# Kernel optimization log

Hardware: AMD Instinct MI355X
Metric: run time of the kernel (lower is better)

Reference implementation:

```python
import jax, jax.numpy as jnp
import numpy as np
from jax import lax

N, XD, L, D, R = 32768, 8, 16, 64, 64
HID_E, HID_N, MIX = 256, 512, 32
LOG2PI = float(np.log(2.0 * np.pi))


def setup_inputs() -> dict:
    key = jax.random.key(0)
    ks = jax.random.split(key, 18)
    g = lambda k, shape, s: (jax.random.normal(k, shape, jnp.float32) * s)
    init_std = 0.001
    return {
        "X": jax.random.normal(ks[0], (N, XD, L), jnp.float32),
        "init_w": g(ks[1], (1, R), init_std),
        "cores": g(ks[2], (L, R, D, R), init_std),          # core_list stacked
        "enc1_w": g(ks[3], (HID_E, XD), 1.0 / np.sqrt(XD)),
        "enc1_b": jnp.zeros((HID_E,), jnp.float32),
        "enc2_w": g(ks[4], (D, HID_E), 1.0 / np.sqrt(HID_E)),
        "enc2_b": jnp.zeros((D,), jnp.float32),
        "nade_w1": g(ks[5], (HID_N, R), 1.0 / np.sqrt(R)),
        "nade_b1": jnp.zeros((HID_N,), jnp.float32),
        "nade_w2": g(ks[6], (R, HID_N), 1.0 / np.sqrt(HID_N)),
        "nade_b2": jnp.zeros((R,), jnp.float32),
        "mu_w": g(ks[7], (MIX * XD, R), 1.0 / np.sqrt(R)),
        "mu_b": jnp.zeros((MIX * XD,), jnp.float32),
        "sig_w": g(ks[8], (MIX * XD, R), 1.0 / np.sqrt(R)),
        "sig_b": jnp.zeros((MIX * XD,), jnp.float32),
        "alpha_w": g(ks[9], (MIX, R), 1.0 / np.sqrt(R)),
        "alpha_b": jnp.zeros((MIX,), jnp.float32),
    }


def _encode(x, enc1_w, enc1_b, enc2_w, enc2_b):
    # x: [..., xd] -> [..., d]  (NADE-style input encoder)
    h = jax.nn.relu(x @ enc1_w.T + enc1_b)
    return h @ enc2_w.T + enc2_b


def _phi(x, h, nade_w1, nade_b1, nade_w2, nade_b2,
         mu_w, mu_b, sig_w, sig_b, alpha_w, alpha_b):
    # x: [n, xd], h: [n, r] hidden state -> [n] mixture-of-Gaussians log-density
    n = x.shape[0]
    h = jax.nn.relu(h @ nade_w1.T + nade_b1)
    h = jax.nn.relu(h @ nade_w2.T + nade_b2)
    mu = (h @ mu_w.T + mu_b).reshape(n, MIX, XD)
    log_sig = (h @ sig_w.T + sig_b).reshape(n, MIX, XD)
    sig = jnp.exp(log_sig)
    log_alpha = jax.nn.log_softmax(h @ alpha_w.T + alpha_b, axis=-1)  # [n, MIX]
    z = (x[:, None, :] - mu) / sig
    comp_lp = jnp.sum(-0.5 * z * z - log_sig - 0.5 * LOG2PI, axis=-1)  # [n, MIX]
    return jax.nn.logsumexp(log_alpha + comp_lp, axis=-1)


def reference(X, init_w, cores, enc1_w, enc1_b, enc2_w, enc2_b,
              nade_w1, nade_b1, nade_w2, nade_b2,
              mu_w, mu_b, sig_w, sig_b, alpha_w, alpha_b):
    n = X.shape[0]
    xseq = jnp.transpose(X, (2, 0, 1))                      # [L, n, xd]
    enc_all = _encode(xseq, enc1_w, enc1_b, enc2_w, enc2_b)  # [L, n, d]
    phi = lambda x, h: _phi(x, h, nade_w1, nade_b1, nade_w2, nade_b2,
                            mu_w, mu_b, sig_w, sig_b, alpha_w, alpha_b)

    tmp0 = jnp.broadcast_to(init_w, (n, R))
    res0 = phi(xseq[0], tmp0)
    norm0 = jnp.sum(tmp0 * tmp0)

    def step(tmp, inp):
        enc_prev, core_prev, x_cur = inp
        tmp = jnp.einsum('nd,ni,idj->nj', enc_prev, tmp, core_prev)
        return tmp, (phi(x_cur, tmp), jnp.sum(tmp * tmp))

    xs = (enc_all[:L - 1], cores[:L - 1], xseq[1:])
    _, (res_steps, norm_steps) = lax.scan(step, tmp0, xs)
    result = res0 + jnp.sum(res_steps, axis=0)   # [n] log-likelihood
    norm = norm0 + jnp.sum(norm_steps)           # scalar Frobenius norm accumulator
    return result, norm
```

## Files before the change

### kernel.cpp

```cpp
#include <hip/hip_runtime.h>

typedef unsigned short u16;
typedef unsigned int u32;
typedef __attribute__((ext_vector_type(8))) __bf16 bf16x8;
typedef __attribute__((ext_vector_type(4))) float f32x4;

#define NSAMP 32768
#define HALF_LOG2PI 0.91893853320467274f

#define O_W1N 0
#define O_W2N 32768
#define O_MUW 65536
#define O_SGW 81920
#define O_ALW 98304
#define O_E1W 100352
#define O_E2W 108544
#define O_CORT 124928
#define CORT_STEP 262144

#define L_TMP 0
#define L_ENC 8192
#define L_H1A 24576
#define L_H1B 32768
#define L_CLP 24576
#define L_ALP 32768
#define L_H2  40960
#define L_LM1 40960
#define L_LM2 41984
#define L_LS1 43008
#define L_LS2 44032
#define L_XP  49152
#define LDS_BYTES 53248

static __device__ __forceinline__ u16 f2b(float x){ return __builtin_bit_cast(u16,(__bf16)x); }
static __device__ __forceinline__ float b2f(u16 u){ return __builtin_bit_cast(float,((u32)u)<<16); }
static __device__ __forceinline__ float b2flo(u32 v){ return __builtin_bit_cast(float, v<<16); }
static __device__ __forceinline__ float b2fhi(u32 v){ return __builtin_bit_cast(float, v & 0xffff0000u); }
static __device__ __forceinline__ u32 pk2(float lo, float hi){
  return (u32)__builtin_bit_cast(u16,(__bf16)lo) | ((u32)__builtin_bit_cast(u16,(__bf16)hi)<<16);
}
static __device__ __forceinline__ f32x4 MF(uint4 a, uint4 b, f32x4 c){
  union U{uint4 q; bf16x8 v;};
  U A, B; A.q=a; B.q=b;
  return __builtin_amdgcn_mfma_f32_16x16x32_bf16(A.v, B.v, c, 0, 0, 0);
}

__global__ void prep_w(const float* __restrict__ nw1, const float* __restrict__ nw2,
                       const float* __restrict__ muw, const float* __restrict__ sgw,
                       const float* __restrict__ alw, const float* __restrict__ e1w,
                       const float* __restrict__ e2w, u16* __restrict__ ws,
                       float* __restrict__ out) {
  int idx0 = blockIdx.x * blockDim.x + threadIdx.x;
  int stride = gridDim.x * blockDim.x;
  for (int idx = idx0; idx < 124928; idx += stride) {
    float v;
    if      (idx < 32768)  v = nw1[idx];
    else if (idx < 65536)  v = nw2[idx - 32768];
    else if (idx < 81920)  v = muw[idx - 65536];
    else if (idx < 98304)  v = sgw[idx - 81920];
    else if (idx < 100352) v = alw[idx - 98304];
    else if (idx < 108544) { int j = idx - 100352; int o = j >> 5, k = j & 31;
                             v = (k < 8) ? e1w[o*8 + k] : 0.0f; }
    else                   v = e2w[idx - 108544];
    ws[idx] = f2b(v);
  }
  if (idx0 == 0) out[NSAMP] = 0.0f;
}

__global__ void prep_core(const float* __restrict__ cores, u16* __restrict__ ws) {
  int t = blockIdx.x >> 6, d = blockIdx.x & 63;
  __shared__ float T[64][65];
  for (int idx = threadIdx.x; idx < 4096; idx += 256) {
    int i = idx >> 6, j = idx & 63;
    T[i][j] = cores[((size_t)(t*64 + i)*64 + d)*64 + j];
  }
  __syncthreads();
  u16* dst = ws + O_CORT + (size_t)t*CORT_STEP + (size_t)d*4096;
  for (int idx = threadIdx.x; idx < 4096; idx += 256) {
    int j = idx >> 6, i = idx & 63;
    dst[j*64 + i] = f2b(T[i][j]);
  }
}

__global__ __launch_bounds__(256, 3)
void fused(const float* __restrict__ X, const float* __restrict__ init_w,
           const float* __restrict__ b1e, const float* __restrict__ b2e,
           const float* __restrict__ b1n, const float* __restrict__ b2n,
           const float* __restrict__ mub, const float* __restrict__ sgb,
           const float* __restrict__ alb, const u16* __restrict__ ws,
           float* __restrict__ out) {
  __shared__ __align__(16) char Lp[LDS_BYTES];
  const int tid = threadIdx.x;
  const int w = tid >> 6, l = tid & 63, li = l & 15, g = l >> 4;
  const int e3 = li & 7;
  const int sw = e3 << 4;
  const int n0 = blockIdx.x * 64;
  float res = 0.f, nrm = 0.f;

  for (int idx = tid; idx < 4096; idx += 256) {
    int s = idx >> 6, r = idx & 63;
    *(u16*)(Lp + L_TMP + s*128 + ((2*r) ^ ((s & 7) << 4))) = f2b(init_w[r]);
  }
  { uint4 z = {0,0,0,0};
    *(uint4*)(Lp + L_XP + tid*16) = z; }
  if (tid < 64) { float v = init_w[tid]; nrm += 64.f * v * v; }
  __syncthreads();

  for (int t = 0; t < 16; ++t) {
    for (int idx = tid; idx < 512; idx += 256) {
      int d = idx >> 6, s = idx & 63;
      float x = X[(size_t)(n0 + s)*128 + d*16 + t];
      *(u16*)(Lp + L_XP + s*64 + ((2*d) ^ ((s & 3) << 4))) = f2b(x);
    }

    uint4 Bq0[4], Bq1[4];
#pragma unroll
    for (int st = 0; st < 4; ++st) {
      int s = st*16 + li;
      Bq0[st] = *(const uint4*)(Lp + L_TMP + s*128 + ((16*g) ^ sw));
      Bq1[st] = *(const uint4*)(Lp + L_TMP + s*128 + ((64 + 16*g) ^ sw));
    }

    f32x4 acc2[4];
#pragma unroll
    for (int st = 0; st < 4; ++st) acc2[st] = (f32x4){0.f,0.f,0.f,0.f};
#pragma unroll 1
    for (int p = 0; p <= 8; ++p) {
      if (p < 8) {
        const u16* a0p = ws + O_W1N + (p*64 + w*16 + li)*64 + 8*g;
        uint4 af0 = *(const uint4*)a0p;
        uint4 af1 = *(const uint4*)(a0p + 32);
        float4 bb = *(const float4*)(b1n + p*64 + w*16 + 4*g);
        char* H1b = Lp + ((p & 1) ? L_H1B : L_H1A);
#pragma unroll
        for (int st = 0; st < 4; ++st) {
          int s = st*16 + li;
          f32x4 a1 = (f32x4){0.f,0.f,0.f,0.f};
          a1 = MF(af0, Bq0[st], a1); a1 = MF(af1, Bq1[st], a1);
          float v0 = fmaxf(a1[0] + bb.x, 0.f), v1 = fmaxf(a1[1] + bb.y, 0.f);
          float v2 = fmaxf(a1[2] + bb.z, 0.f), v3 = fmaxf(a1[3] + bb.w, 0.f);
          *(u32*)(H1b + s*128 + ((32*w + 8*g) ^ sw))     = pk2(v0, v1);
          *(u32*)(H1b + s*128 + ((32*w + 8*g + 4) ^ sw)) = pk2(v2, v3);
        }
      }
      if (p > 0) {
        int q = p - 1;
        const u16* a2p = ws + O_W2N + (w*16 + li)*512 + q*64 + 8*g;
        uint4 c0 = *(const uint4*)a2p;
        uint4 c1 = *(const uint4*)(a2p + 32);
        const char* H1r = Lp + ((q & 1) ? L_H1B : L_H1A);
#pragma unroll
        for (int st = 0; st < 4; ++st) {
          int s = st*16 + li;
          uint4 b0 = *(const uint4*)(H1r + s*128 + ((16*g) ^ sw));
          uint4 b1 = *(const uint4*)(H1r + s*128 + ((64 + 16*g) ^ sw));
          acc2[st] = MF(c0, b0, acc2[st]); acc2[st] = MF(c1, b1, acc2[st]);
        }
      }
      __syncthreads();
    }
    {
      float4 bb = *(const float4*)(b2n + w*16 + 4*g);
#pragma unroll
      for (int st = 0; st < 4; ++st) {
        int s = st*16 + li;
        float v0 = fmaxf(acc2[st][0] + bb.x, 0.f), v1 = fmaxf(acc2[st][1] + bb.y, 0.f);
        float v2 = fmaxf(acc2[st][2] + bb.z, 0.f), v3 = fmaxf(acc2[st][3] + bb.w, 0.f);
        *(u32*)(Lp + L_H2 + s*128 + ((32*w + 8*g) ^ sw))     = pk2(v0, v1);
        *(u32*)(Lp + L_H2 + s*128 + ((32*w + 8*g + 4) ^ sw)) = pk2(v2, v3);
      }
    }
    __syncthreads();

    float xv[4][4];
#pragma unroll
    for (int st = 0; st < 4; ++st) {
      int s = st*16 + li;
      uint2 xq = *(const uint2*)(Lp + L_XP + s*64 + ((8*(g & 1)) ^ ((li & 3) << 4)));
      xv[st][0] = b2flo(xq.x); xv[st][1] = b2fhi(xq.x);
      xv[st][2] = b2flo(xq.y); xv[st][3] = b2fhi(xq.y);
    }

#pragma unroll 1
    for (int c = 0; c < 4; ++c) {
      int ob = c*64 + w*16;
      const u16* as_ = ws + O_SGW + (ob + li)*64 + 8*g;
      const u16* am_ = ws + O_MUW + (ob + li)*64 + 8*g;
      uint4 sf0 = *(const uint4*)as_, sf1 = *(const uint4*)(as_ + 32);
      uint4 mf0 = *(const uint4*)am_, mf1 = *(const uint4*)(am_ + 32);
      float4 bs = *(const float4*)(sgb + ob + 4*g);
      float4 bm = *(const float4*)(mub + ob + 4*g);
      const float bsv[4] = {bs.x,bs.y,bs.z,bs.w};
      const float bmv[4] = {bm.x,bm.y,bm.z,bm.w};
#pragma unroll
      for (int st = 0; st < 4; ++st) {
        int s = st*16 + li;
        uint4 b0 = *(const uint4*)(Lp + L_H2 + s*128 + ((16*g) ^ sw));
        uint4 b1 = *(const uint4*)(Lp + L_H2 + s*128 + ((64 + 16*g) ^ sw));
        f32x4 aS = (f32x4){0.f,0.f,0.f,0.f}, aM = (f32x4){0.f,0.f,0.f,0.f};
        aS = MF(sf0, b0, aS); aS = MF(sf1, b1, aS);
        aM = MF(mf0, b0, aM); aM = MF(mf1, b1, aM);
        float part = 0.f;
#pragma unroll
        for (int r = 0; r < 4; ++r) {
          float ls = aS[r] + bsv[r];
          float mu = aM[r] + bmv[r];
          float z = (xv[st][r] - mu) * __expf(-ls);
          part += -0.5f*z*z - ls - HALF_LOG2PI;
        }
        float comb = part + __shfl_xor(part, 16);
        if (!(g & 1)) {
          int mix = c*8 + 2*w + (g >> 1);
          *(float*)(Lp + L_CLP + (mix*64 + s)*4) = comb;
        }
      }
    }
    {
      int s = w*16 + li;
      uint4 b0 = *(const uint4*)(Lp + L_H2 + s*128 + ((16*g) ^ sw));
      uint4 b1 = *(const uint4*)(Lp + L_H2 + s*128 + ((64 + 16*g) ^ sw));
#pragma unroll
      for (int ot = 0; ot < 2; ++ot) {
        const u16* aa = ws + O_ALW + (ot*16 + li)*64 + 8*g;
        uint4 a0 = *(const uint4*)aa, a1 = *(const uint4*)(aa + 32);
        f32x4 acc = (f32x4){0.f,0.f,0.f,0.f};
        acc = MF(a0, b0, acc); acc = MF(a1, b1, acc);
        float4 ab4 = *(const float4*)(alb + ot*16 + 4*g);
        const float abv[4] = {ab4.x, ab4.y, ab4.z, ab4.w};
#pragma unroll
        for (int r = 0; r < 4; ++r)
          *(float*)(Lp + L_ALP + ((ot*16 + 4*g + r)*64 + s)*4) = acc[r] + abv[r];
      }
    }
    __syncthreads();

    float g1, g2;
    {
      int s = l;
      float m1 = -1e30f, m2 = -1e30f;
#pragma unroll
      for (int mm = 0; mm < 8; ++mm) {
        int m = w*8 + mm;
        float a = *(const float*)(Lp + L_ALP + (m*64 + s)*4);
        float c = *(const float*)(Lp + L_CLP + (m*64 + s)*4);
        m1 = fmaxf(m1, a + c); m2 = fmaxf(m2, a);
      }
      *(float*)(Lp + L_LM1 + (w*64 + s)*4) = m1;
      *(float*)(Lp + L_LM2 + (w*64 + s)*4) = m2;
      __syncthreads();
      g1 = fmaxf(fmaxf(*(const float*)(Lp + L_LM1 + s*4),
                       *(const float*)(Lp + L_LM1 + (64 + s)*4)),
                 fmaxf(*(const float*)(Lp + L_LM1 + (128 + s)*4),
                       *(const float*)(Lp + L_LM1 + (192 + s)*4)));
      g2 = fmaxf(fmaxf(*(const float*)(Lp + L_LM2 + s*4),
                       *(const float*)(Lp + L_LM2 + (64 + s)*4)),
                 fmaxf(*(const float*)(Lp + L_LM2 + (128 + s)*4),
                       *(const float*)(Lp + L_LM2 + (192 + s)*4)));
      float s1 = 0.f, s2 = 0.f;
#pragma unroll
      for (int mm = 0; mm < 8; ++mm) {
        int m = w*8 + mm;
        float a = *(const float*)(Lp + L_ALP + (m*64 + s)*4);
        float c = *(const float*)(Lp + L_CLP + (m*64 + s)*4);
        s1 += __expf(a + c - g1); s2 += __expf(a - g2);
      }
      *(float*)(Lp + L_LS1 + (w*64 + s)*4) = s1;
      *(float*)(Lp + L_LS2 + (w*64 + s)*4) = s2;
      __syncthreads();
    }
    if (tid < 64) {
      float s1 = *(const float*)(Lp + L_LS1 + tid*4)
               + *(const float*)(Lp + L_LS1 + (64 + tid)*4)
               + *(const float*)(Lp + L_LS1 + (128 + tid)*4)
               + *(const float*)(Lp + L_LS1 + (192 + tid)*4);
      float s2 = *(const float*)(Lp + L_LS2 + tid*4)
               + *(const float*)(Lp + L_LS2 + (64 + tid)*4)
               + *(const float*)(Lp + L_LS2 + (128 + tid)*4)
               + *(const float*)(Lp + L_LS2 + (192 + tid)*4);
      res += (g1 + __logf(s1)) - (g2 + __logf(s2));
    }
    if (t == 15) break;
    __syncthreads();

    f32x4 acE[4];
#pragma unroll
    for (int st = 0; st < 4; ++st) acE[st] = (f32x4){0.f,0.f,0.f,0.f};
#pragma unroll 1
    for (int p = 0; p <= 4; ++p) {
      if (p < 4) {
        const u16* aep = ws + O_E1W + (p*64 + w*16 + li)*32 + 8*g;
        uint4 ae = *(const uint4*)aep;
        float4 bb = *(const float4*)(b1e + p*64 + w*16 + 4*g);
        char* H1b = Lp + ((p & 1) ? L_H1B : L_H1A);
#pragma unroll
        for (int st = 0; st < 4; ++st) {
          int s = st*16 + li;
          uint4 b0 = *(const uint4*)(Lp + L_XP + s*64 + ((16*g) ^ ((s & 3) << 4)));
          f32x4 ah = (f32x4){0.f,0.f,0.f,0.f};
          ah = MF(ae, b0, ah);
          float v0 = fmaxf(ah[0] + bb.x, 0.f), v1 = fmaxf(ah[1] + bb.y, 0.f);
          float v2 = fmaxf(ah[2] + bb.z, 0.f), v3 = fmaxf(ah[3] + bb.w, 0.f);
          *(u32*)(H1b + s*128 + ((32*w + 8*g) ^ sw))     = pk2(v0, v1);
          *(u32*)(H1b + s*128 + ((32*w + 8*g + 4) ^ sw)) = pk2(v2, v3);
        }
      }
      if (p > 0) {
        int q = p - 1;
        const u16* c0p = ws + O_E2W + (w*16 + li)*256 + q*64 + 8*g;
        uint4 c0 = *(const uint4*)c0p, c1 = *(const uint4*)(c0p + 32);
        const char* H1r = Lp + ((q & 1) ? L_H1B : L_H1A);
#pragma unroll
        for (int st = 0; st < 4; ++st) {
          int s = st*16 + li;
          uint4 b0 = *(const uint4*)(H1r + s*128 + ((16*g) ^ sw));
          uint4 b1 = *(const uint4*)(H1r + s*128 + ((64 + 16*g) ^ sw));
          acE[st] = MF(c0, b0, acE[st]); acE[st] = MF(c1, b1, acE[st]);
        }
      }
      if (p == 4) {
        float4 be = *(const float4*)(b2e + w*16 + 4*g);
        const float bev[4] = {be.x, be.y, be.z, be.w};
#pragma unroll
        for (int st = 0; st < 4; ++st) {
          int s = st*16 + li;
#pragma unroll
          for (int r = 0; r < 4; ++r) {
            int d = w*16 + 4*g + r;
            *(float*)(Lp + L_ENC + s*256 + ((((d >> 3) ^ e3)) << 5) + ((d & 7) << 2))
                = acE[st][r] + bev[r];
          }
        }
      }
      __syncthreads();
    }

    f32x4 acc[4];
#pragma unroll
    for (int st = 0; st < 4; ++st) acc[st] = (f32x4){0.f,0.f,0.f,0.f};
    const u16* AJ = ws + O_CORT + (size_t)t*CORT_STEP + (size_t)(w*16 + li)*64 + 8*g;
    uint4 Ac0 = *(const uint4*)(AJ);
    uint4 Ac1 = *(const uint4*)(AJ + 32);
#pragma unroll 1
    for (int dg = 0; dg < 16; ++dg) {
      f32x4 E[4];
#pragma unroll
      for (int st = 0; st < 4; ++st)
        E[st] = *(const f32x4*)(Lp + L_ENC + (st*16 + li)*256 +
                                (((dg >> 1) ^ e3) << 5) + ((dg & 1) << 4));
#pragma unroll
      for (int dd = 0; dd < 4; ++dd) {
        uint4 An0 = Ac0, An1 = Ac1;
        if (dd < 3 || dg < 15) {
          const u16* ap = AJ + (size_t)(dg*4 + dd + 1)*4096;
          An0 = *(const uint4*)(ap);
          An1 = *(const uint4*)(ap + 32);
        }
        __builtin_amdgcn_s_setprio(1);
#pragma unroll
        for (int st = 0; st < 4; ++st) {
          f32x4 y = (f32x4){0.f,0.f,0.f,0.f};
          y = MF(Ac0, Bq0[st], y);
          y = MF(Ac1, Bq1[st], y);
          float e = E[st][dd];
          acc[st][0] += e * y[0]; acc[st][1] += e * y[1];
          acc[st][2] += e * y[2]; acc[st][3] += e * y[3];
        }
        __builtin_amdgcn_s_setprio(0);
        Ac0 = An0; Ac1 = An1;
      }
    }
#pragma unroll
    for (int st = 0; st < 4; ++st) {
      int s = st*16 + li;
      nrm += acc[st][0]*acc[st][0] + acc[st][1]*acc[st][1]
           + acc[st][2]*acc[st][2] + acc[st][3]*acc[st][3];
      uint2 pv;
      pv.x = pk2(acc[st][0], acc[st][1]);
      pv.y = pk2(acc[st][2], acc[st][3]);
      *(uint2*)(Lp + L_TMP + s*128 + ((32*w + 8*g) ^ sw)) = pv;
    }
    __syncthreads();
  }

  if (tid < 64) out[n0 + tid] = res;

  __syncthreads();
  *(float*)(Lp + L_H1A + tid*4) = nrm;
  __syncthreads();
  if (tid < 64) {
    float v = *(const float*)(Lp + L_H1A + tid*4)
            + *(const float*)(Lp + L_H1A + (tid + 64)*4)
            + *(const float*)(Lp + L_H1A + (tid + 128)*4)
            + *(const float*)(Lp + L_H1A + (tid + 192)*4);
#pragma unroll
    for (int off = 32; off > 0; off >>= 1) v += __shfl_down(v, off);
    if (tid == 0) atomicAdd(out + NSAMP, v);
  }
}

extern "C" void kernel_launch(void* const* d_in, const int* in_sizes, int n_in,
                              void* d_out, int out_size, void* d_ws, size_t ws_size,
                              hipStream_t stream) {
  const float* X      = (const float*)d_in[0];
  const float* init_w = (const float*)d_in[1];
  const float* cores  = (const float*)d_in[2];
  const float* e1w    = (const float*)d_in[3];
  const float* b1e    = (const float*)d_in[4];
  const float* e2w    = (const float*)d_in[5];
  const float* b2e    = (const float*)d_in[6];
  const float* nw1    = (const float*)d_in[7];
  const float* b1n    = (const float*)d_in[8];
  const float* nw2    = (const float*)d_in[9];
  const float* b2n    = (const float*)d_in[10];
  const float* muw    = (const float*)d_in[11];
  const float* mub    = (const float*)d_in[12];
  const float* sgw    = (const float*)d_in[13];
  const float* sgb    = (const float*)d_in[14];
  const float* alw    = (const float*)d_in[15];
  const float* alb    = (const float*)d_in[16];
  float* out = (float*)d_out;
  u16*   ws  = (u16*)d_ws;

  prep_w<<<64, 256, 0, stream>>>(nw1, nw2, muw, sgw, alw, e1w, e2w, ws, out);
  prep_core<<<960, 256, 0, stream>>>(cores, ws);
  fused<<<NSAMP/64, 256, 0, stream>>>(X, init_w, b1e, b2e, b1n, b2n,
                                      mub, sgb, alb, ws, out);
}
```

Before: 906.0 us.

## Split fused block across 8 waves, halving per-wave sample tiles

Doubles the block to 512 threads so each of 8 waves handles 32 samples (half the sample tiles) instead of 64, with waves split by output slice and sample half. Alpha weights and biases are hoisted out of the time loop into registers. The core contraction loop now double-buffers core fragments two steps ahead and prefetches the next encoder chunk. This raises wave-level parallelism and latency hiding, but each core fragment is now loaded by twice as many waves and the reductions span more partial rows.

```diff
diff --git a/kernel.cpp b/kernel.cpp
--- a/kernel.cpp
+++ b/kernel.cpp
@@ -26,9 +26,9 @@
 #define L_ALP 32768
 #define L_H2  40960
 #define L_LM1 40960
-#define L_LM2 41984
-#define L_LS1 43008
-#define L_LS2 44032
+#define L_LM2 43008
+#define L_LS1 45056
+#define L_LS2 47104
 #define L_XP  49152
 #define LDS_BYTES 53248
 
@@ -82,7 +82,7 @@
   }
 }
 
-__global__ __launch_bounds__(256, 3)
+__global__ __launch_bounds__(512, 4)
 void fused(const float* __restrict__ X, const float* __restrict__ init_w,
            const float* __restrict__ b1e, const float* __restrict__ b2e,
            const float* __restrict__ b1n, const float* __restrict__ b2n,
@@ -92,98 +92,106 @@
   __shared__ __align__(16) char Lp[LDS_BYTES];
   const int tid = threadIdx.x;
   const int w = tid >> 6, l = tid & 63, li = l & 15, g = l >> 4;
+  const int wo = w & 3, wh = w >> 2;
   const int e3 = li & 7;
   const int sw = e3 << 4;
   const int n0 = blockIdx.x * 64;
   float res = 0.f, nrm = 0.f;
 
-  for (int idx = tid; idx < 4096; idx += 256) {
+  uint4 aw0, aw1; float4 ab4;
+  {
+    const u16* aa = ws + O_ALW + (wh*16 + li)*64 + 8*g;
+    aw0 = *(const uint4*)aa; aw1 = *(const uint4*)(aa + 32);
+    ab4 = *(const float4*)(alb + wh*16 + 4*g);
+  }
+  const float4 b2nv = *(const float4*)(b2n + wo*16 + 4*g);
+  const float4 b2ev = *(const float4*)(b2e + wo*16 + 4*g);
+
+  for (int idx = tid; idx < 4096; idx += 512) {
     int s = idx >> 6, r = idx & 63;
     *(u16*)(Lp + L_TMP + s*128 + ((2*r) ^ ((s & 7) << 4))) = f2b(init_w[r]);
   }
-  { uint4 z = {0,0,0,0};
-    *(uint4*)(Lp + L_XP + tid*16) = z; }
+  if (tid < 256) { uint4 z = {0,0,0,0}; *(uint4*)(Lp + L_XP + tid*16) = z; }
   if (tid < 64) { float v = init_w[tid]; nrm += 64.f * v * v; }
   __syncthreads();
 
   for (int t = 0; t < 16; ++t) {
-    for (int idx = tid; idx < 512; idx += 256) {
-      int d = idx >> 6, s = idx & 63;
+    {
+      int d = tid >> 6, s = tid & 63;
       float x = X[(size_t)(n0 + s)*128 + d*16 + t];
       *(u16*)(Lp + L_XP + s*64 + ((2*d) ^ ((s & 3) << 4))) = f2b(x);
     }
 
-    uint4 Bq0[4], Bq1[4];
-#pragma unroll
-    for (int st = 0; st < 4; ++st) {
-      int s = st*16 + li;
-      Bq0[st] = *(const uint4*)(Lp + L_TMP + s*128 + ((16*g) ^ sw));
-      Bq1[st] = *(const uint4*)(Lp + L_TMP + s*128 + ((64 + 16*g) ^ sw));
-    }
-
-    f32x4 acc2[4];
-#pragma unroll
-    for (int st = 0; st < 4; ++st) acc2[st] = (f32x4){0.f,0.f,0.f,0.f};
+    uint4 Bq0[2], Bq1[2];
+#pragma unroll
+    for (int stl = 0; stl < 2; ++stl) {
+      int s = wh*32 + stl*16 + li;
+      Bq0[stl] = *(const uint4*)(Lp + L_TMP + s*128 + ((16*g) ^ sw));
+      Bq1[stl] = *(const uint4*)(Lp + L_TMP + s*128 + ((64 + 16*g) ^ sw));
+    }
+
+    f32x4 acc2[2];
+#pragma unroll
+    for (int stl = 0; stl < 2; ++stl) acc2[stl] = (f32x4){0.f,0.f,0.f,0.f};
 #pragma unroll 1
     for (int p = 0; p <= 8; ++p) {
       if (p < 8) {
-        const u16* a0p = ws + O_W1N + (p*64 + w*16 + li)*64 + 8*g;
+        const u16* a0p = ws + O_W1N + (p*64 + wo*16 + li)*64 + 8*g;
         uint4 af0 = *(const uint4*)a0p;
         uint4 af1 = *(const uint4*)(a0p + 32);
-        float4 bb = *(const float4*)(b1n + p*64 + w*16 + 4*g);
+        float4 bb = *(const float4*)(b1n + p*64 + wo*16 + 4*g);
         char* H1b = Lp + ((p & 1) ? L_H1B : L_H1A);
 #pragma unroll
-        for (int st = 0; st < 4; ++st) {
-          int s = st*16 + li;
+        for (int stl = 0; stl < 2; ++stl) {
+          int s = wh*32 + stl*16 + li;
           f32x4 a1 = (f32x4){0.f,0.f,0.f,0.f};
-          a1 = MF(af0, Bq0[st], a1); a1 = MF(af1, Bq1[st], a1);
+          a1 = MF(af0, Bq0[stl], a1); a1 = MF(af1, Bq1[stl], a1);
           float v0 = fmaxf(a1[0] + bb.x, 0.f), v1 = fmaxf(a1[1] + bb.y, 0.f);
           float v2 = fmaxf(a1[2] + bb.z, 0.f), v3 = fmaxf(a1[3] + bb.w, 0.f);
-          *(u32*)(H1b + s*128 + ((32*w + 8*g) ^ sw))     = pk2(v0, v1);
-          *(u32*)(H1b + s*128 + ((32*w + 8*g + 4) ^ sw)) = pk2(v2, v3);
+          *(u32*)(H1b + s*128 + ((32*wo + 8*g) ^ sw))     = pk2(v0, v1);
+          *(u32*)(H1b + s*128 + ((32*wo + 8*g + 4) ^ sw)) = pk2(v2, v3);
         }
       }
       if (p > 0) {
         int q = p - 1;
-        const u16* a2p = ws + O_W2N + (w*16 + li)*512 + q*64 + 8*g;
+        const u16* a2p = ws + O_W2N + (wo*16 + li)*512 + q*64 + 8*g;
         uint4 c0 = *(const uint4*)a2p;
         uint4 c1 = *(const uint4*)(a2p + 32);
         const char* H1r = Lp + ((q & 1) ? L_H1B : L_H1A);
 #pragma unroll
-        for (int st = 0; st < 4; ++st) {
-          int s = st*16 + li;
+        for (int stl = 0; stl < 2; ++stl) {
+          int s = wh*32 + stl*16 + li;
           uint4 b0 = *(const uint4*)(H1r + s*128 + ((16*g) ^ sw));
           uint4 b1 = *(const uint4*)(H1r + s*128 + ((64 + 16*g) ^ sw));
-          acc2[st] = MF(c0, b0, acc2[st]); acc2[st] = MF(c1, b1, acc2[st]);
+          acc2[stl] = MF(c0, b0, acc2[stl]); acc2[stl] = MF(c1, b1, acc2[stl]);
         }
       }
       __syncthreads();
     }
     {
-      float4 bb = *(const float4*)(b2n + w*16 + 4*g);
-#pragma unroll
-      for (int st = 0; st < 4; ++st) {
-        int s = st*16 + li;
-        float v0 = fmaxf(acc2[st][0] + bb.x, 0.f), v1 = fmaxf(acc2[st][1] + bb.y, 0.f);
-        float v2 = fmaxf(acc2[st][2] + bb.z, 0.f), v3 = fmaxf(acc2[st][3] + bb.w, 0.f);
-        *(u32*)(Lp + L_H2 + s*128 + ((32*w + 8*g) ^ sw))     = pk2(v0, v1);
-        *(u32*)(Lp + L_H2 + s*128 + ((32*w + 8*g + 4) ^ sw)) = pk2(v2, v3);
+#pragma unroll
+      for (int stl = 0; stl < 2; ++stl) {
+        int s = wh*32 + stl*16 + li;
+        float v0 = fmaxf(acc2[stl][0] + b2nv.x, 0.f), v1 = fmaxf(acc2[stl][1] + b2nv.y, 0.f);
+        float v2 = fmaxf(acc2[stl][2] + b2nv.z, 0.f), v3 = fmaxf(acc2[stl][3] + b2nv.w, 0.f);
+        *(u32*)(Lp + L_H2 + s*128 + ((32*wo + 8*g) ^ sw))     = pk2(v0, v1);
+        *(u32*)(Lp + L_H2 + s*128 + ((32*wo + 8*g + 4) ^ sw)) = pk2(v2, v3);
       }
     }
     __syncthreads();
 
-    float xv[4][4];
-#pragma unroll
-    for (int st = 0; st < 4; ++st) {
-      int s = st*16 + li;
+    float xv[2][4];
+#pragma unroll
+    for (int stl = 0; stl < 2; ++stl) {
+      int s = wh*32 + stl*16 + li;
       uint2 xq = *(const uint2*)(Lp + L_XP + s*64 + ((8*(g & 1)) ^ ((li & 3) << 4)));
-      xv[st][0] = b2flo(xq.x); xv[st][1] = b2fhi(xq.x);
-      xv[st][2] = b2flo(xq.y); xv[st][3] = b2fhi(xq.y);
+      xv[stl][0] = b2flo(xq.x); xv[stl][1] = b2fhi(xq.x);
+      xv[stl][2] = b2flo(xq.y); xv[stl][3] = b2fhi(xq.y);
     }
 
 #pragma unroll 1
     for (int c = 0; c < 4; ++c) {
-      int ob = c*64 + w*16;
+      int ob = c*64 + wo*16;
       const u16* as_ = ws + O_SGW + (ob + li)*64 + 8*g;
       const u16* am_ = ws + O_MUW + (ob + li)*64 + 8*g;
       uint4 sf0 = *(const uint4*)as_, sf1 = *(const uint4*)(as_ + 32);
@@ -193,8 +201,8 @@
       const float bsv[4] = {bs.x,bs.y,bs.z,bs.w};
       const float bmv[4] = {bm.x,bm.y,bm.z,bm.w};
 #pragma unroll
-      for (int st = 0; st < 4; ++st) {
-        int s = st*16 + li;
+      for (int stl = 0; stl < 2; ++stl) {
+        int s = wh*32 + stl*16 + li;
         uint4 b0 = *(const uint4*)(Lp + L_H2 + s*128 + ((16*g) ^ sw));
         uint4 b1 = *(const uint4*)(Lp + L_H2 + s*128 + ((64 + 16*g) ^ sw));
         f32x4 aS = (f32x4){0.f,0.f,0.f,0.f}, aM = (f32x4){0.f,0.f,0.f,0.f};
@@ -205,32 +213,26 @@
         for (int r = 0; r < 4; ++r) {
           float ls = aS[r] + bsv[r];
           float mu = aM[r] + bmv[r];
-          float z = (xv[st][r] - mu) * __expf(-ls);
+          float z = (xv[stl][r] - mu) * __expf(-ls);
           part += -0.5f*z*z - ls - HALF_LOG2PI;
         }
         float comb = part + __shfl_xor(part, 16);
         if (!(g & 1)) {
-          int mix = c*8 + 2*w + (g >> 1);
+          int mix = c*8 + 2*wo + (g >> 1);
           *(float*)(Lp + L_CLP + (mix*64 + s)*4) = comb;
         }
       }
     }
     {
-      int s = w*16 + li;
+      int s = wo*16 + li;
       uint4 b0 = *(const uint4*)(Lp + L_H2 + s*128 + ((16*g) ^ sw));
       uint4 b1 = *(const uint4*)(Lp + L_H2 + s*128 + ((64 + 16*g) ^ sw));
-#pragma unroll
-      for (int ot = 0; ot < 2; ++ot) {
-        const u16* aa = ws + O_ALW + (ot*16 + li)*64 + 8*g;
-        uint4 a0 = *(const uint4*)aa, a1 = *(const uint4*)(aa + 32);
-        f32x4 acc = (f32x4){0.f,0.f,0.f,0.f};
-        acc = MF(a0, b0, acc); acc = MF(a1, b1, acc);
-        float4 ab4 = *(const float4*)(alb + ot*16 + 4*g);
-        const float abv[4] = {ab4.x, ab4.y, ab4.z, ab4.w};
-#pragma unroll
-        for (int r = 0; r < 4; ++r)
-          *(float*)(Lp + L_ALP + ((ot*16 + 4*g + r)*64 + s)*4) = acc[r] + abv[r];
-      }
+      f32x4 acc = (f32x4){0.f,0.f,0.f,0.f};
+      acc = MF(aw0, b0, acc); acc = MF(aw1, b1, acc);
+      const float abv[4] = {ab4.x, ab4.y, ab4.z, ab4.w};
+#pragma unroll
+      for (int r = 0; r < 4; ++r)
+        *(float*)(Lp + L_ALP + ((wh*16 + 4*g + r)*64 + s)*4) = acc[r] + abv[r];
     }
     __syncthreads();
 
@@ -239,8 +241,8 @@
       int s = l;
       float m1 = -1e30f, m2 = -1e30f;
 #pragma unroll
-      for (int mm = 0; mm < 8; ++mm) {
-        int m = w*8 + mm;
+      for (int mm = 0; mm < 4; ++mm) {
+        int m = w*4 + mm;
         float a = *(const float*)(Lp + L_ALP + (m*64 + s)*4);
         float c = *(const float*)(Lp + L_CLP + (m*64 + s)*4);
         m1 = fmaxf(m1, a + c); m2 = fmaxf(m2, a);
@@ -248,18 +250,16 @@
       *(float*)(Lp + L_LM1 + (w*64 + s)*4) = m1;
       *(float*)(Lp + L_LM2 + (w*64 + s)*4) = m2;
       __syncthreads();
-      g1 = fmaxf(fmaxf(*(const float*)(Lp + L_LM1 + s*4),
-                       *(const float*)(Lp + L_LM1 + (64 + s)*4)),
-                 fmaxf(*(const float*)(Lp + L_LM1 + (128 + s)*4),
-                       *(const float*)(Lp + L_LM1 + (192 + s)*4)));
-      g2 = fmaxf(fmaxf(*(const float*)(Lp + L_LM2 + s*4),
-                       *(const float*)(Lp + L_LM2 + (64 + s)*4)),
-                 fmaxf(*(const float*)(Lp + L_LM2 + (128 + s)*4),
-                       *(const float*)(Lp + L_LM2 + (192 + s)*4)));
+      g1 = -1e30f; g2 = -1e30f;
+#pragma unroll
+      for (int k = 0; k < 8; ++k) {
+        g1 = fmaxf(g1, *(const float*)(Lp + L_LM1 + (k*64 + s)*4));
+        g2 = fmaxf(g2, *(const float*)(Lp + L_LM2 + (k*64 + s)*4));
+      }
       float s1 = 0.f, s2 = 0.f;
 #pragma unroll
-      for (int mm = 0; mm < 8; ++mm) {
-        int m = w*8 + mm;
+      for (int mm = 0; mm < 4; ++mm) {
+        int m = w*4 + mm;
         float a = *(const float*)(Lp + L_ALP + (m*64 + s)*4);
         float c = *(const float*)(Lp + L_CLP + (m*64 + s)*4);
         s1 += __expf(a + c - g1); s2 += __expf(a - g2);
@@ -269,115 +269,128 @@
       __syncthreads();
     }
     if (tid < 64) {
-      float s1 = *(const float*)(Lp + L_LS1 + tid*4)
-               + *(const float*)(Lp + L_LS1 + (64 + tid)*4)
-               + *(const float*)(Lp + L_LS1 + (128 + tid)*4)
-               + *(const float*)(Lp + L_LS1 + (192 + tid)*4);
-      float s2 = *(const float*)(Lp + L_LS2 + tid*4)
-               + *(const float*)(Lp + L_LS2 + (64 + tid)*4)
-               + *(const float*)(Lp + L_LS2 + (128 + tid)*4)
-               + *(const float*)(Lp + L_LS2 + (192 + tid)*4);
+      float s1 = 0.f, s2 = 0.f;
+#pragma unroll
+      for (int k = 0; k < 8; ++k) {
+        s1 += *(const float*)(Lp + L_LS1 + (k*64 + tid)*4);
+        s2 += *(const float*)(Lp + L_LS2 + (k*64 + tid)*4);
+      }
       res += (g1 + __logf(s1)) - (g2 + __logf(s2));
     }
     if (t == 15) break;
     __syncthreads();
 
-    f32x4 acE[4];
-#pragma unroll
-    for (int st = 0; st < 4; ++st) acE[st] = (f32x4){0.f,0.f,0.f,0.f};
+    f32x4 acE[2];
+#pragma unroll
+    for (int stl = 0; stl < 2; ++stl) acE[stl] = (f32x4){0.f,0.f,0.f,0.f};
 #pragma unroll 1
     for (int p = 0; p <= 4; ++p) {
       if (p < 4) {
-        const u16* aep = ws + O_E1W + (p*64 + w*16 + li)*32 + 8*g;
+        const u16* aep = ws + O_E1W + (p*64 + wo*16 + li)*32 + 8*g;
         uint4 ae = *(const uint4*)aep;
-        float4 bb = *(const float4*)(b1e + p*64 + w*16 + 4*g);
+        float4 be1 = *(const float4*)(b1e + p*64 + wo*16 + 4*g);
         char* H1b = Lp + ((p & 1) ? L_H1B : L_H1A);
 #pragma unroll
-        for (int st = 0; st < 4; ++st) {
-          int s = st*16 + li;
+        for (int stl = 0; stl < 2; ++stl) {
+          int s = wh*32 + stl*16 + li;
           uint4 b0 = *(const uint4*)(Lp + L_XP + s*64 + ((16*g) ^ ((s & 3) << 4)));
           f32x4 ah = (f32x4){0.f,0.f,0.f,0.f};
           ah = MF(ae, b0, ah);
-          float v0 = fmaxf(ah[0] + bb.x, 0.f), v1 = fmaxf(ah[1] + bb.y, 0.f);
-          float v2 = fmaxf(ah[2] + bb.z, 0.f), v3 = fmaxf(ah[3] + bb.w, 0.f);
-          *(u32*)(H1b + s*128 + ((32*w + 8*g) ^ sw))     = pk2(v0, v1);
-          *(u32*)(H1b + s*128 + ((32*w + 8*g + 4) ^ sw)) = pk2(v2, v3);
+          float v0 = fmaxf(ah[0] + be1.x, 0.f), v1 = fmaxf(ah[1] + be1.y, 0.f);
+          float v2 = fmaxf(ah[2] + be1.z, 0.f), v3 = fmaxf(ah[3] + be1.w, 0.f);
+          *(u32*)(H1b + s*128 + ((32*wo + 8*g) ^ sw))     = pk2(v0, v1);
+          *(u32*)(H1b + s*128 + ((32*wo + 8*g + 4) ^ sw)) = pk2(v2, v3);
         }
       }
       if (p > 0) {
         int q = p - 1;
-        const u16* c0p = ws + O_E2W + (w*16 + li)*256 + q*64 + 8*g;
+        const u16* c0p = ws + O_E2W + (wo*16 + li)*256 + q*64 + 8*g;
         uint4 c0 = *(const uint4*)c0p, c1 = *(const uint4*)(c0p + 32);
         const char* H1r = Lp + ((q & 1) ? L_H1B : L_H1A);
 #pragma unroll
-        for (int st = 0; st < 4; ++st) {
-          int s = st*16 + li;
+        for (int stl = 0; stl < 2; ++stl) {
+          int s = wh*32 + stl*16 + li;
           uint4 b0 = *(const uint4*)(H1r + s*128 + ((16*g) ^ sw));
           uint4 b1 = *(const uint4*)(H1r + s*128 + ((64 + 16*g) ^ sw));
-          acE[st] = MF(c0, b0, acE[st]); acE[st] = MF(c1, b1, acE[st]);
+          acE[stl] = MF(c0, b0, acE[stl]); acE[stl] = MF(c1, b1, acE[stl]);
         }
       }
       if (p == 4) {
-        float4 be = *(const float4*)(b2e + w*16 + 4*g);
-        const float bev[4] = {be.x, be.y, be.z, be.w};
-#pragma unroll
-        for (int st = 0; st < 4; ++st) {
-          int s = st*16 + li;
+        const float bev[4] = {b2ev.x, b2ev.y, b2ev.z, b2ev.w};
+#pragma unroll
+        for (int stl = 0; stl < 2; ++stl) {
+          int s = wh*32 + stl*16 + li;
 #pragma unroll
           for (int r = 0; r < 4; ++r) {
-            int d = w*16 + 4*g + r;
+            int d = wo*16 + 4*g + r;
             *(float*)(Lp + L_ENC + s*256 + ((((d >> 3) ^ e3)) << 5) + ((d & 7) << 2))
-                = acE[st][r] + bev[r];
+                = acE[stl][r] + bev[r];
           }
         }
       }
       __syncthreads();
     }
 
-    f32x4 acc[4];
-#pragma unroll
-    for (int st = 0; st < 4; ++st) acc[st] = (f32x4){0.f,0.f,0.f,0.f};
-    const u16* AJ = ws + O_CORT + (size_t)t*CORT_STEP + (size_t)(w*16 + li)*64 + 8*g;
-    uint4 Ac0 = *(const uint4*)(AJ);
-    uint4 Ac1 = *(const uint4*)(AJ + 32);
+    f32x4 acc[2];
+#pragma unroll
+    for (int stl = 0; stl < 2; ++stl) acc[stl] = (f32x4){0.f,0.f,0.f,0.f};
+    const u16* AJ = ws + O_CORT + (size_t)t*CORT_STEP + (size_t)(wo*16 + li)*64 + 8*g;
+    uint4 A0[2], A1[2];
+#pragma unroll
+    for (int sl = 0; sl < 2; ++sl) {
+      const u16* ap = AJ + (size_t)sl*4096;
+      A0[sl] = *(const uint4*)(ap);
+      A1[sl] = *(const uint4*)(ap + 32);
+    }
+    f32x4 Ec[2], En[2];
+#pragma unroll
+    for (int stl = 0; stl < 2; ++stl) {
+      int s = wh*32 + stl*16 + li;
+      Ec[stl] = *(const f32x4*)(Lp + L_ENC + s*256 + (e3 << 5));
+    }
 #pragma unroll 1
-    for (int dg = 0; dg < 16; ++dg) {
-      f32x4 E[4];
-#pragma unroll
-      for (int st = 0; st < 4; ++st)
-        E[st] = *(const f32x4*)(Lp + L_ENC + (st*16 + li)*256 +
-                                (((dg >> 1) ^ e3) << 5) + ((dg & 1) << 4));
+    for (int dq = 0; dq < 16; ++dq) {
+      if (dq < 15) {
+#pragma unroll
+        for (int stl = 0; stl < 2; ++stl) {
+          int s = wh*32 + stl*16 + li;
+          En[stl] = *(const f32x4*)(Lp + L_ENC + s*256 +
+                     ((((dq+1) >> 1) ^ e3) << 5) + (((dq+1) & 1) << 4));
+        }
+      }
 #pragma unroll
       for (int dd = 0; dd < 4; ++dd) {
-        uint4 An0 = Ac0, An1 = Ac1;
-        if (dd < 3 || dg < 15) {
-          const u16* ap = AJ + (size_t)(dg*4 + dd + 1)*4096;
-          An0 = *(const uint4*)(ap);
-          An1 = *(const uint4*)(ap + 32);
-        }
+        int dk = dq*4 + dd;
+        int sl = dk & 1;
         __builtin_amdgcn_s_setprio(1);
 #pragma unroll
-        for (int st = 0; st < 4; ++st) {
+        for (int stl = 0; stl < 2; ++stl) {
           f32x4 y = (f32x4){0.f,0.f,0.f,0.f};
-          y = MF(Ac0, Bq0[st], y);
-          y = MF(Ac1, Bq1[st], y);
-          float e = E[st][dd];
-          acc[st][0] += e * y[0]; acc[st][1] += e * y[1];
-          acc[st][2] += e * y[2]; acc[st][3] += e * y[3];
+          y = MF(A0[sl], Bq0[stl], y);
+          y = MF(A1[sl], Bq1[stl], y);
+          float e = Ec[stl][dd];
+          acc[stl][0] += e * y[0]; acc[stl][1] += e * y[1];
+          acc[stl][2] += e * y[2]; acc[stl][3] += e * y[3];
         }
         __builtin_amdgcn_s_setprio(0);
-        Ac0 = An0; Ac1 = An1;
-      }
-    }
-#pragma unroll
-    for (int st = 0; st < 4; ++st) {
-      int s = st*16 + li;
-      nrm += acc[st][0]*acc[st][0] + acc[st][1]*acc[st][1]
-           + acc[st][2]*acc[st][2] + acc[st][3]*acc[st][3];
+        if (dk + 2 < 64) {
+          const u16* ap = AJ + (size_t)(dk + 2)*4096;
+          A0[sl] = *(const uint4*)(ap);
+          A1[sl] = *(const uint4*)(ap + 32);
+        }
+      }
+#pragma unroll
+      for (int stl = 0; stl < 2; ++stl) Ec[stl] = En[stl];
+    }
+#pragma unroll
+    for (int stl = 0; stl < 2; ++stl) {
+      int s = wh*32 + stl*16 + li;
+      nrm += acc[stl][0]*acc[stl][0] + acc[stl][1]*acc[stl][1]
+           + acc[stl][2]*acc[stl][2] + acc[stl][3]*acc[stl][3];
       uint2 pv;
-      pv.x = pk2(acc[st][0], acc[st][1]);
-      pv.y = pk2(acc[st][2], acc[st][3]);
-      *(uint2*)(Lp + L_TMP + s*128 + ((32*w + 8*g) ^ sw)) = pv;
+      pv.x = pk2(acc[stl][0], acc[stl][1]);
+      pv.y = pk2(acc[stl][2], acc[stl][3]);
+      *(uint2*)(Lp + L_TMP + s*128 + ((32*wo + 8*g) ^ sw)) = pv;
     }
     __syncthreads();
   }
@@ -388,10 +401,10 @@
   *(float*)(Lp + L_H1A + tid*4) = nrm;
   __syncthreads();
   if (tid < 64) {
-    float v = *(const float*)(Lp + L_H1A + tid*4)
-            + *(const float*)(Lp + L_H1A + (tid + 64)*4)
-            + *(const float*)(Lp + L_H1A + (tid + 128)*4)
-            + *(const float*)(Lp + L_H1A + (tid + 192)*4);
+    float v = 0.f;
+#pragma unroll
+    for (int k = 0; k < 8; ++k)
+      v += *(const float*)(Lp + L_H1A + (k*64 + tid)*4);
 #pragma unroll
     for (int off = 32; off > 0; off >>= 1) v += __shfl_down(v, off);
     if (tid == 0) atomicAdd(out + NSAMP, v);
@@ -423,6 +436,6 @@
 
   prep_w<<<64, 256, 0, stream>>>(nw1, nw2, muw, sgw, alw, e1w, e2w, ws, out);
   prep_core<<<960, 256, 0, stream>>>(cores, ws);
-  fused<<<NSAMP/64, 256, 0, stream>>>(X, init_w, b1e, b2e, b1n, b2n,
+  fused<<<NSAMP/64, 512, 0, stream>>>(X, init_w, b1e, b2e, b1n, b2n,
                                       mub, sgb, alb, ws, out);
 }
```

After: 1.490 ms. 64.4% more time.
